# Optimization experiments

Measured on AMD Instinct MI355X. Metric: run time of the kernel, lower is better.

Reference implementation:

```python
import jax, jax.numpy as jnp
import numpy as np

IN_DIM = 128
OUT_DIM = 128
B, N = 8, 2048
NEG_SLOPE = 0.2


def setup_inputs() -> dict:
    key = jax.random.key(0)
    k_h, k_adj, k_W, k_a = jax.random.split(key, 4)
    h = jax.random.normal(k_h, (B, N, IN_DIM), dtype=jnp.float32)
    adj = jax.random.randint(k_adj, (B, N, N), 0, 2, dtype=jnp.int32)
    # nn.Linear(in, out, bias=False): weight [out, in]
    W = jax.random.normal(k_W, (OUT_DIM, IN_DIM), dtype=jnp.float32) * (1.0 / np.sqrt(IN_DIM))
    # nn.Linear(2*out, 1, bias=False): weight [1, 2*out] -> store as vector [2*out]
    a = jax.random.normal(k_a, (2 * OUT_DIM,), dtype=jnp.float32) * (1.0 / np.sqrt(2 * OUT_DIM))
    return {"h": h, "adj": adj, "W": W, "a": a}


def reference(h, adj, W, a):
    # Wh: [B, N, Fo]
    Wh = jnp.einsum("bnf,of->bno", h, W)
    Fo = Wh.shape[-1]
    a_src, a_dst = a[:Fo], a[Fo:]
    # attn(cat([Wh_i, Wh_j])) == (Wh_i . a_src) + (Wh_j . a_dst) -- avoids [B,N,N,2F]
    s = Wh @ a_src  # [B, N]
    t = Wh @ a_dst  # [B, N]
    e = jax.nn.leaky_relu(s[:, :, None] + t[:, None, :], negative_slope=NEG_SLOPE)  # [B,N,N]
    e = jnp.where(adj == 0, -jnp.inf, e)
    alpha = jax.nn.softmax(e, axis=-1)
    alpha = jnp.nan_to_num(alpha, nan=0.0)  # rows with no neighbors -> 0
    return jnp.einsum("bnm,bmo->bno", alpha, Wh)
```

## Files before the change

kernel.cpp:

```cpp
#include <hip/hip_runtime.h>
#include <hip/hip_bf16.h>
#include <hip/hip_fp16.h>
#include <math.h>

#define B_ 8
#define N_ 2048
#define F_ 128

typedef __attribute__((ext_vector_type(8))) _Float16 half8;
typedef __attribute__((ext_vector_type(4))) float f32x4;

__global__ __launch_bounds__(256) void k_mask(
    const int* __restrict__ adj, unsigned long long* __restrict__ mask)
{
    const int wv = threadIdx.x >> 6, lane = threadIdx.x & 63;
    const int row = blockIdx.x * 4 + wv;
    const int* ap = adj + ((size_t)row << 11);
    unsigned long long* mp = mask + (size_t)row * 32;
    #pragma unroll
    for (int it0 = 0; it0 < 32; it0 += 8) {
        int v[8];
        #pragma unroll
        for (int u = 0; u < 8; ++u) v[u] = ap[(it0 + u) * 64 + lane];
        #pragma unroll
        for (int u = 0; u < 8; ++u) {
            unsigned long long bm = __ballot(v[u] != 0);
            if (lane == 0) mp[it0 + u] = bm;
        }
    }
}

__global__ __launch_bounds__(256) void k_gemm(
    const float* __restrict__ h, const float* __restrict__ W,
    const float* __restrict__ a,
    _Float16* __restrict__ WhH, float* __restrict__ sv, float* __restrict__ tv)
{
    __shared__ float h_s[64][129];
    __shared__ float Wt[128][68];
    __shared__ float wsm[128], wtm[128];
    __shared__ float sred[64][4], tred[64][4];

    const int t = threadIdx.x;
    const int rowblk = blockIdx.x >> 1;
    const int ohalf  = blockIdx.x & 1;
    const int r0 = rowblk * 64;

    {
        const int f = (t & 31) * 4;
        #pragma unroll
        for (int it = 0; it < 8; ++it) {
            const int r = (t >> 5) + it * 8;
            float4 v = *(const float4*)&h[(size_t)(r0 + r) * F_ + f];
            h_s[r][f] = v.x; h_s[r][f + 1] = v.y;
            h_s[r][f + 2] = v.z; h_s[r][f + 3] = v.w;
        }
    }
    {
        const int f = (t & 31) * 4;
        #pragma unroll
        for (int it = 0; it < 8; ++it) {
            const int o = (t >> 5) + it * 8;
            float4 v = *(const float4*)&W[(size_t)(ohalf * 64 + o) * F_ + f];
            Wt[f][o] = v.x; Wt[f + 1][o] = v.y;
            Wt[f + 2][o] = v.z; Wt[f + 3][o] = v.w;
        }
    }
    {
        const int f = t & 127;
        const int which = t >> 7;
        const float* av = a + which * 128;
        float acc = 0.f;
        for (int o = 0; o < 128; ++o)
            acc += W[(size_t)o * F_ + f] * av[o];
        if (which == 0) wsm[f] = acc; else wtm[f] = acc;
    }
    __syncthreads();

    const int o4 = t & 15;
    const int r4 = t >> 4;
    float acc[4][4];
    #pragma unroll
    for (int i = 0; i < 4; ++i)
        #pragma unroll
        for (int j = 0; j < 4; ++j) acc[i][j] = 0.f;

    #pragma unroll 4
    for (int k = 0; k < 128; ++k) {
        float4 w = *(const float4*)&Wt[k][o4 * 4];
        float h0 = h_s[r4 * 4 + 0][k];
        float h1 = h_s[r4 * 4 + 1][k];
        float h2 = h_s[r4 * 4 + 2][k];
        float h3 = h_s[r4 * 4 + 3][k];
        acc[0][0] += h0 * w.x; acc[0][1] += h0 * w.y; acc[0][2] += h0 * w.z; acc[0][3] += h0 * w.w;
        acc[1][0] += h1 * w.x; acc[1][1] += h1 * w.y; acc[1][2] += h1 * w.z; acc[1][3] += h1 * w.w;
        acc[2][0] += h2 * w.x; acc[2][1] += h2 * w.y; acc[2][2] += h2 * w.z; acc[2][3] += h2 * w.w;
        acc[3][0] += h3 * w.x; acc[3][1] += h3 * w.y; acc[3][2] += h3 * w.z; acc[3][3] += h3 * w.w;
    }

    {
        const int Rbase = r0 + r4 * 4;
        const int b    = Rbase >> 11;
        const int jj   = Rbase & 2047;
        const int jblk = jj >> 5;
        const int k8   = (jj >> 3) & 3;
        const int kk   = jj & 7;
        #pragma unroll
        for (int jo = 0; jo < 4; ++jo) {
            const int o = ohalf * 64 + o4 * 4 + jo;
            size_t off = ((size_t)(b * 64 + jblk) * 128 + o) * 32 + k8 * 8 + kk;
            union { _Float16 x[4]; uint2 u; } pk;
            pk.x[0] = (_Float16)acc[0][jo];
            pk.x[1] = (_Float16)acc[1][jo];
            pk.x[2] = (_Float16)acc[2][jo];
            pk.x[3] = (_Float16)acc[3][jo];
            *(uint2*)(WhH + off) = pk.u;
        }
    }

    {
        const int r = t & 63, part = t >> 6;
        float as_ = 0.f, at_ = 0.f;
        const int kb = part * 32;
        for (int k = kb; k < kb + 32; ++k) {
            float hv = h_s[r][k];
            as_ += hv * wsm[k];
            at_ += hv * wtm[k];
        }
        sred[r][part] = as_; tred[r][part] = at_;
    }
    __syncthreads();
    if (ohalf == 0 && t < 64) {
        sv[r0 + t] = sred[t][0] + sred[t][1] + sred[t][2] + sred[t][3];
        tv[r0 + t] = tred[t][0] + tred[t][1] + tred[t][2] + tred[t][3];
    }
}

__global__ __launch_bounds__(256, 2) void k_attn(
    const _Float16* __restrict__ WhH, const float* __restrict__ sv,
    const float* __restrict__ tv, const unsigned int* __restrict__ maskd,
    float* __restrict__ out)
{
    __shared__ float redO[4][32][128];
    __shared__ float redL[4][32];
    __shared__ float tmr[4];

    const int t  = threadIdx.x;
    const int b  = blockIdx.x & 7;
    const int i0 = (blockIdx.x >> 3) * 32;
    const float* tb = tv + ((size_t)b << 11);

    float tm = -INFINITY;
    #pragma unroll
    for (int k = 0; k < 8; ++k) tm = fmaxf(tm, tb[t + k * 256]);
    #pragma unroll
    for (int k = 32; k; k >>= 1) tm = fmaxf(tm, __shfl_xor(tm, k, 64));
    if ((t & 63) == 0) tmr[t >> 6] = tm;
    __syncthreads();
    const float tmax = fmaxf(fmaxf(tmr[0], tmr[1]), fmaxf(tmr[2], tmr[3]));

    const int wv   = t >> 6;
    const int lane = t & 63;
    const int m_   = lane & 15;
    const int q_   = lane >> 4;

    const float s0 = sv[((size_t)b << 11) + i0 + m_];
    const float s1 = sv[((size_t)b << 11) + i0 + 16 + m_];
    const float M0 = fmaxf(s0 + tmax, 0.f);
    const float M1 = fmaxf(s1 + tmax, 0.f);

    const unsigned int* mrow0 =
        maskd + (size_t)(((b << 11) + i0 + m_)) * 64 + wv * 16;
    const unsigned int* mrow1 = mrow0 + 16 * 64;
    const float* tq = tb + wv * 512 + q_ * 8;
    const _Float16* wbase = WhH + (((size_t)b * 64 + wv * 16) << 12)
                          + (size_t)m_ * 32 + q_ * 8;

    f32x4 acc0[8], acc1[8];
    #pragma unroll
    for (int n = 0; n < 8; ++n) {
        acc0[n] = (f32x4){0.f, 0.f, 0.f, 0.f};
        acc1[n] = (f32x4){0.f, 0.f, 0.f, 0.f};
    }
    float lsum0 = 0.f, lsum1 = 0.f;

    unsigned int mc0 = mrow0[0], mc1 = mrow1[0];

    for (int jj = 0; jj < 16; ++jj) {
        const int nxt = (jj + 1) & 15;
        unsigned int mn0 = mrow0[nxt];
        unsigned int mn1 = mrow1[nxt];

        const _Float16* wb = wbase + ((size_t)jj << 12);
        half8 bf[8];
        #pragma unroll
        for (int n = 0; n < 8; ++n)
            bf[n] = *(const half8*)(wb + n * 512);

        float4 tL = *(const float4*)&tq[jj * 32];
        float4 tH = *(const float4*)&tq[jj * 32 + 4];
        const unsigned int bq0 = mc0 >> (q_ * 8);
        const unsigned int bq1 = mc1 >> (q_ * 8);

        float tvk[8] = {tL.x, tL.y, tL.z, tL.w, tH.x, tH.y, tH.z, tH.w};
        half8 af0, af1;
        #pragma unroll
        for (int k = 0; k < 8; ++k) {
            float e0 = s0 + tvk[k]; e0 = fmaxf(e0, 0.2f * e0);
            float p0 = (bq0 >> k) & 1 ? __expf(e0 - M0) : 0.f;
            float e1 = s1 + tvk[k]; e1 = fmaxf(e1, 0.2f * e1);
            float p1 = (bq1 >> k) & 1 ? __expf(e1 - M1) : 0.f;
            lsum0 += p0; lsum1 += p1;
            af0[k] = (_Float16)p0; af1[k] = (_Float16)p1;
        }

        #pragma unroll
        for (int n = 0; n < 8; ++n) {
            acc0[n] = __builtin_amdgcn_mfma_f32_16x16x32_f16(af0, bf[n], acc0[n], 0, 0, 0);
            acc1[n] = __builtin_amdgcn_mfma_f32_16x16x32_f16(af1, bf[n], acc1[n], 0, 0, 0);
        }
        mc0 = mn0; mc1 = mn1;
    }

    lsum0 += __shfl_xor(lsum0, 16, 64); lsum0 += __shfl_xor(lsum0, 32, 64);
    lsum1 += __shfl_xor(lsum1, 16, 64); lsum1 += __shfl_xor(lsum1, 32, 64);
    if (q_ == 0) { redL[wv][m_] = lsum0; redL[wv][16 + m_] = lsum1; }

    #pragma unroll
    for (int n = 0; n < 8; ++n)
        #pragma unroll
        for (int r = 0; r < 4; ++r) {
            redO[wv][q_ * 4 + r][n * 16 + m_]      = acc0[n][r];
            redO[wv][16 + q_ * 4 + r][n * 16 + m_] = acc1[n][r];
        }
    __syncthreads();

    {
        const int row = t >> 3;
        const int c0  = (t & 7) * 16;
        const float li = redL[0][row] + redL[1][row] + redL[2][row] + redL[3][row];
        const float sc = li > 0.f ? 1.f / li : 0.f;
        float* op = out + (((size_t)((b << 11) + i0 + row)) << 7) + c0;
        #pragma unroll
        for (int c = 0; c < 16; ++c) {
            float v = redO[0][row][c0 + c] + redO[1][row][c0 + c]
                    + redO[2][row][c0 + c] + redO[3][row][c0 + c];
            op[c] = v * sc;
        }
    }
}

extern "C" void kernel_launch(void* const* d_in, const int* in_sizes, int n_in,
                              void* d_out, int out_size, void* d_ws, size_t ws_size,
                              hipStream_t stream) {
    const float* h   = (const float*)d_in[0];
    const int*   adj = (const int*)d_in[1];
    const float* W   = (const float*)d_in[2];
    const float* a   = (const float*)d_in[3];
    float* out = (float*)d_out;

    _Float16* WhH = (_Float16*)d_ws;
    float* sv = (float*)((char*)d_ws + (size_t)4 * 1024 * 1024);
    float* tv = sv + (size_t)B_ * N_;
    unsigned long long* mask =
        (unsigned long long*)((char*)d_ws + (size_t)4 * 1024 * 1024 + 256 * 1024);

    k_mask<<<4096, 256, 0, stream>>>(adj, mask);
    k_gemm<<<512, 256, 0, stream>>>(h, W, a, WhH, sv, tv);
    k_attn<<<512, 256, 0, stream>>>(WhH, sv, tv, (const unsigned int*)mask, out);
}
```

Baseline: 248.0 us.

## Fuse adjacency mask read into attention kernel and factor exponentials

```diff
diff --git a/kernel.cpp b/kernel.cpp
--- a/kernel.cpp
+++ b/kernel.cpp
@@ -9,26 +9,6 @@
 
 typedef __attribute__((ext_vector_type(8))) _Float16 half8;
 typedef __attribute__((ext_vector_type(4))) float f32x4;
-
-__global__ __launch_bounds__(256) void k_mask(
-    const int* __restrict__ adj, unsigned long long* __restrict__ mask)
-{
-    const int wv = threadIdx.x >> 6, lane = threadIdx.x & 63;
-    const int row = blockIdx.x * 4 + wv;
-    const int* ap = adj + ((size_t)row << 11);
-    unsigned long long* mp = mask + (size_t)row * 32;
-    #pragma unroll
-    for (int it0 = 0; it0 < 32; it0 += 8) {
-        int v[8];
-        #pragma unroll
-        for (int u = 0; u < 8; ++u) v[u] = ap[(it0 + u) * 64 + lane];
-        #pragma unroll
-        for (int u = 0; u < 8; ++u) {
-            unsigned long long bm = __ballot(v[u] != 0);
-            if (lane == 0) mp[it0 + u] = bm;
-        }
-    }
-}
 
 __global__ __launch_bounds__(256) void k_gemm(
     const float* __restrict__ h, const float* __restrict__ W,
@@ -137,43 +117,59 @@
 
 __global__ __launch_bounds__(256, 2) void k_attn(
     const _Float16* __restrict__ WhH, const float* __restrict__ sv,
-    const float* __restrict__ tv, const unsigned int* __restrict__ maskd,
+    const float* __restrict__ tv, const int* __restrict__ adj,
     float* __restrict__ out)
 {
-    __shared__ float redO[4][32][128];
-    __shared__ float redL[4][32];
-    __shared__ float tmr[4];
+    __shared__ float  redO[4][16][128];
+    __shared__ float  redL[4][32];
+    __shared__ float2 efS[2048];
+    __shared__ float  tmr[4];
 
     const int t  = threadIdx.x;
     const int b  = blockIdx.x & 7;
     const int i0 = (blockIdx.x >> 3) * 32;
     const float* tb = tv + ((size_t)b << 11);
 
+    float tv8[8];
     float tm = -INFINITY;
     #pragma unroll
-    for (int k = 0; k < 8; ++k) tm = fmaxf(tm, tb[t + k * 256]);
+    for (int k = 0; k < 8; ++k) {
+        tv8[k] = tb[t + k * 256];
+        tm = fmaxf(tm, tv8[k]);
+    }
     #pragma unroll
     for (int k = 32; k; k >>= 1) tm = fmaxf(tm, __shfl_xor(tm, k, 64));
     if ((t & 63) == 0) tmr[t >> 6] = tm;
     __syncthreads();
     const float tmax = fmaxf(fmaxf(tmr[0], tmr[1]), fmaxf(tmr[2], tmr[3]));
+
+    #pragma unroll
+    for (int k = 0; k < 8; ++k) {
+        float d = tv8[k] - tmax;
+        efS[t + k * 256] = make_float2(__expf(d), __expf(0.2f * d));
+    }
 
     const int wv   = t >> 6;
     const int lane = t & 63;
     const int m_   = lane & 15;
     const int q_   = lane >> 4;
-
-    const float s0 = sv[((size_t)b << 11) + i0 + m_];
-    const float s1 = sv[((size_t)b << 11) + i0 + 16 + m_];
+    const int jbase = wv * 512;
+
+    const int girow0 = (b << 11) + i0 + m_;
+    const int girow1 = girow0 + 16;
+    const float s0 = sv[girow0];
+    const float s1 = sv[girow1];
     const float M0 = fmaxf(s0 + tmax, 0.f);
     const float M1 = fmaxf(s1 + tmax, 0.f);
-
-    const unsigned int* mrow0 =
-        maskd + (size_t)(((b << 11) + i0 + m_)) * 64 + wv * 16;
-    const unsigned int* mrow1 = mrow0 + 16 * 64;
-    const float* tq = tb + wv * 512 + q_ * 8;
-    const _Float16* wbase = WhH + (((size_t)b * 64 + wv * 16) << 12)
-                          + (size_t)m_ * 32 + q_ * 8;
+    const float C0 = __expf(s0 + tmax - M0), D0 = __expf(0.2f * (s0 + tmax) - M0);
+    const float C1 = __expf(s1 + tmax - M1), D1 = __expf(0.2f * (s1 + tmax) - M1);
+    const float T0 = __expf(-s0 - tmax);
+    const float T1 = __expf(-s1 - tmax);
+
+    const int* arow0 = adj + ((size_t)girow0 << 11) + jbase + q_ * 8;
+    const int* arow1 = adj + ((size_t)girow1 << 11) + jbase + q_ * 8;
+    const _Float16* whc = WhH + (((size_t)b * 64 + wv * 16) << 12)
+                        + (size_t)m_ * 32 + q_ * 8;
 
     f32x4 acc0[8], acc1[8];
     #pragma unroll
@@ -183,32 +179,37 @@
     }
     float lsum0 = 0.f, lsum1 = 0.f;
 
-    unsigned int mc0 = mrow0[0], mc1 = mrow1[0];
+    __syncthreads();
+
+    int4 a0L = *(const int4*)(arow0), a0H = *(const int4*)(arow0 + 4);
+    int4 a1L = *(const int4*)(arow1), a1H = *(const int4*)(arow1 + 4);
 
     for (int jj = 0; jj < 16; ++jj) {
         const int nxt = (jj + 1) & 15;
-        unsigned int mn0 = mrow0[nxt];
-        unsigned int mn1 = mrow1[nxt];
-
-        const _Float16* wb = wbase + ((size_t)jj << 12);
+        int4 n0L = *(const int4*)(arow0 + nxt * 32);
+        int4 n0H = *(const int4*)(arow0 + nxt * 32 + 4);
+        int4 n1L = *(const int4*)(arow1 + nxt * 32);
+        int4 n1H = *(const int4*)(arow1 + nxt * 32 + 4);
+
+        const _Float16* wb = whc + ((size_t)jj << 12);
         half8 bf[8];
         #pragma unroll
-        for (int n = 0; n < 8; ++n)
-            bf[n] = *(const half8*)(wb + n * 512);
-
-        float4 tL = *(const float4*)&tq[jj * 32];
-        float4 tH = *(const float4*)&tq[jj * 32 + 4];
-        const unsigned int bq0 = mc0 >> (q_ * 8);
-        const unsigned int bq1 = mc1 >> (q_ * 8);
-
-        float tvk[8] = {tL.x, tL.y, tL.z, tL.w, tH.x, tH.y, tH.z, tH.w};
+        for (int n = 0; n < 8; ++n) bf[n] = *(const half8*)(wb + n * 512);
+
+        const float4* efp = (const float4*)&efS[jbase + jj * 32 + q_ * 8];
+        float4 v0 = efp[0], v1 = efp[1], v2 = efp[2], v3 = efp[3];
+        float Ek[8] = {v0.x, v0.z, v1.x, v1.z, v2.x, v2.z, v3.x, v3.z};
+        float Fk[8] = {v0.y, v0.w, v1.y, v1.w, v2.y, v2.w, v3.y, v3.w};
+        int  a0k[8] = {a0L.x, a0L.y, a0L.z, a0L.w, a0H.x, a0H.y, a0H.z, a0H.w};
+        int  a1k[8] = {a1L.x, a1L.y, a1L.z, a1L.w, a1H.x, a1H.y, a1H.z, a1H.w};
+
         half8 af0, af1;
         #pragma unroll
         for (int k = 0; k < 8; ++k) {
-            float e0 = s0 + tvk[k]; e0 = fmaxf(e0, 0.2f * e0);
-            float p0 = (bq0 >> k) & 1 ? __expf(e0 - M0) : 0.f;
-            float e1 = s1 + tvk[k]; e1 = fmaxf(e1, 0.2f * e1);
-            float p1 = (bq1 >> k) & 1 ? __expf(e1 - M1) : 0.f;
+            float p0 = (Ek[k] > T0) ? C0 * Ek[k] : D0 * Fk[k];
+            p0 = a0k[k] ? p0 : 0.f;
+            float p1 = (Ek[k] > T1) ? C1 * Ek[k] : D1 * Fk[k];
+            p1 = a1k[k] ? p1 : 0.f;
             lsum0 += p0; lsum1 += p1;
             af0[k] = (_Float16)p0; af1[k] = (_Float16)p1;
         }
@@ -218,34 +219,46 @@
             acc0[n] = __builtin_amdgcn_mfma_f32_16x16x32_f16(af0, bf[n], acc0[n], 0, 0, 0);
             acc1[n] = __builtin_amdgcn_mfma_f32_16x16x32_f16(af1, bf[n], acc1[n], 0, 0, 0);
         }
-        mc0 = mn0; mc1 = mn1;
+        a0L = n0L; a0H = n0H; a1L = n1L; a1H = n1H;
     }
 
     lsum0 += __shfl_xor(lsum0, 16, 64); lsum0 += __shfl_xor(lsum0, 32, 64);
     lsum1 += __shfl_xor(lsum1, 16, 64); lsum1 += __shfl_xor(lsum1, 32, 64);
     if (q_ == 0) { redL[wv][m_] = lsum0; redL[wv][16 + m_] = lsum1; }
-
-    #pragma unroll
-    for (int n = 0; n < 8; ++n)
-        #pragma unroll
-        for (int r = 0; r < 4; ++r) {
-            redO[wv][q_ * 4 + r][n * 16 + m_]      = acc0[n][r];
-            redO[wv][16 + q_ * 4 + r][n * 16 + m_] = acc1[n][r];
-        }
-    __syncthreads();
-
-    {
-        const int row = t >> 3;
-        const int c0  = (t & 7) * 16;
-        const float li = redL[0][row] + redL[1][row] + redL[2][row] + redL[3][row];
-        const float sc = li > 0.f ? 1.f / li : 0.f;
-        float* op = out + (((size_t)((b << 11) + i0 + row)) << 7) + c0;
-        #pragma unroll
-        for (int c = 0; c < 16; ++c) {
-            float v = redO[0][row][c0 + c] + redO[1][row][c0 + c]
-                    + redO[2][row][c0 + c] + redO[3][row][c0 + c];
-            op[c] = v * sc;
-        }
+    __syncthreads();
+
+    #pragma unroll
+    for (int half = 0; half < 2; ++half) {
+        #pragma unroll
+        for (int n = 0; n < 8; ++n)
+            #pragma unroll
+            for (int r = 0; r < 4; ++r)
+                redO[wv][q_ * 4 + r][n * 16 + m_] =
+                    half ? acc1[n][r] : acc0[n][r];
+        __syncthreads();
+        {
+            const int rr  = t >> 4;
+            const int c0  = (t & 15) * 8;
+            const int row = half * 16 + rr;
+            const float li = redL[0][row] + redL[1][row]
+                           + redL[2][row] + redL[3][row];
+            const float sc = li > 0.f ? 1.f / li : 0.f;
+            float4 vA, vB;
+            vA.x = redO[0][rr][c0]     + redO[1][rr][c0]     + redO[2][rr][c0]     + redO[3][rr][c0];
+            vA.y = redO[0][rr][c0 + 1] + redO[1][rr][c0 + 1] + redO[2][rr][c0 + 1] + redO[3][rr][c0 + 1];
+            vA.z = redO[0][rr][c0 + 2] + redO[1][rr][c0 + 2] + redO[2][rr][c0 + 2] + redO[3][rr][c0 + 2];
+            vA.w = redO[0][rr][c0 + 3] + redO[1][rr][c0 + 3] + redO[2][rr][c0 + 3] + redO[3][rr][c0 + 3];
+            vB.x = redO[0][rr][c0 + 4] + redO[1][rr][c0 + 4] + redO[2][rr][c0 + 4] + redO[3][rr][c0 + 4];
+            vB.y = redO[0][rr][c0 + 5] + redO[1][rr][c0 + 5] + redO[2][rr][c0 + 5] + redO[3][rr][c0 + 5];
+            vB.z = redO[0][rr][c0 + 6] + redO[1][rr][c0 + 6] + redO[2][rr][c0 + 6] + redO[3][rr][c0 + 6];
+            vB.w = redO[0][rr][c0 + 7] + redO[1][rr][c0 + 7] + redO[2][rr][c0 + 7] + redO[3][rr][c0 + 7];
+            float* op = out + (((size_t)((b << 11) + i0 + row)) << 7) + c0;
+            float4 oA = {vA.x * sc, vA.y * sc, vA.z * sc, vA.w * sc};
+            float4 oB = {vB.x * sc, vB.y * sc, vB.z * sc, vB.w * sc};
+            *(float4*)op       = oA;
+            *(float4*)(op + 4) = oB;
+        }
+        __syncthreads();
     }
 }
 
@@ -258,13 +271,11 @@
     const float* a   = (const float*)d_in[3];
     float* out = (float*)d_out;
 
-    _Float16* WhH = (_Float16*)d_ws;
-    float* sv = (float*)((char*)d_ws + (size_t)4 * 1024 * 1024);
+    char* ws = (char*)d_ws;
+    _Float16* WhH = (_Float16*)ws;
+    float* sv = (float*)(ws + (size_t)4 * 1024 * 1024);
     float* tv = sv + (size_t)B_ * N_;
-    unsigned long long* mask =
-        (unsigned long long*)((char*)d_ws + (size_t)4 * 1024 * 1024 + 256 * 1024);
-
-    k_mask<<<4096, 256, 0, stream>>>(adj, mask);
+
     k_gemm<<<512, 256, 0, stream>>>(h, W, a, WhH, sv, tv);
-    k_attn<<<512, 256, 0, stream>>>(WhH, sv, tv, (const unsigned int*)mask, out);
+    k_attn<<<512, 256, 0, stream>>>(WhH, sv, tv, adj, out);
 }
```

Result: faster. 225.1 us (median of 2 runs) (-9.2%).
